# Performance work log

Measured on AMD Instinct MI355X. Metric: run time of the kernel, lower is better.

The kernel has to match this reference:

```python
import jax, jax.numpy as jnp
import numpy as np
from jax import lax

IMG = 224.0
IOU_THRESH = 0.5

def box_cxcywh_to_xyxy(b):
    cx, cy, w, h = b[..., 0], b[..., 1], b[..., 2], b[..., 3]
    return jnp.stack([cx - 0.5 * w, cy - 0.5 * h, cx + 0.5 * w, cy + 0.5 * h], axis=-1)

def box_iou(a, b):
    area_a = (a[:, 2] - a[:, 0]) * (a[:, 3] - a[:, 1])
    area_b = (b[:, 2] - b[:, 0]) * (b[:, 3] - b[:, 1])
    lt = jnp.maximum(a[:, None, :2], b[None, :, :2])
    rb = jnp.minimum(a[:, None, 2:], b[None, :, 2:])
    wh = jnp.clip(rb - lt, 0.0)
    inter = wh[..., 0] * wh[..., 1]
    return inter / (area_a[:, None] + area_b[None, :] - inter)

def gumbel_softmax(key, logits, axis, tau=1.0):
    # straight-through hard gumbel-softmax (matches torch hard=True)
    g = jax.random.gumbel(key, logits.shape, logits.dtype)
    y = jax.nn.softmax((logits + g) / tau, axis=axis)
    y_hard = jax.nn.one_hot(jnp.argmax(y, axis=axis), y.shape[axis], axis=axis, dtype=y.dtype)
    return y + lax.stop_gradient(y_hard - y)

def nms_indices(boxes, scores, thresh):
    # iterative greedy NMS, returns kept indices in descending-score order (as torchvision)
    n = boxes.shape[0]
    order = jnp.argsort(-scores)
    b = boxes[order]
    areas = (b[:, 2] - b[:, 0]) * (b[:, 3] - b[:, 1])
    pos = jnp.arange(n)
    def body(i, suppressed):
        bi = b[i]
        lt = jnp.maximum(bi[:2], b[:, :2])
        rb = jnp.minimum(bi[2:], b[:, 2:])
        wh = jnp.clip(rb - lt, 0.0)
        inter = wh[:, 0] * wh[:, 1]
        iou = inter / (areas[i] + areas - inter)
        sup = (iou > thresh) & (pos > i) & jnp.logical_not(suppressed[i])
        return suppressed | sup
    suppressed = lax.fori_loop(0, n, body, jnp.zeros((n,), bool))
    keep = np.asarray(jnp.logical_not(suppressed))
    return jnp.asarray(np.asarray(order)[keep])

def _keys():
    return jax.random.split(jax.random.key(42), 3)

def _boxes_and_scores(classencodings, pred_logits, pred_boxes, tgt_ids, batch_idx, tgt_bbox, k0):
    C = classencodings.shape[0]
    B, Q, D = pred_logits.shape
    similarity = jnp.einsum('bqd,cd->bqc', pred_logits, classencodings)
    out_scores = jnp.max(similarity, axis=-1)
    clt = gumbel_softmax(k0, similarity, axis=-1)                      # [B,Q,C] hard
    offx = jnp.arange(C, dtype=pred_logits.dtype) * IMG
    offy = jnp.arange(B, dtype=pred_logits.dtype) * IMG
    ox = jnp.sum(clt * offx, axis=-1)                                  # [B,Q]
    oy = jnp.broadcast_to(offy[:, None], (B, Q))
    out_off = jnp.tile(jnp.stack([ox, oy], axis=-1), (1, 1, 2))        # [B,Q,4]
    out_bbox = (box_cxcywh_to_xyxy(pred_boxes) + out_off).reshape(-1, 4)
    f = pred_logits.dtype
    gt_off = jnp.tile(jnp.stack([IMG * tgt_ids.astype(f), IMG * batch_idx.astype(f)], axis=-1), (1, 2))
    tb = box_cxcywh_to_xyxy(tgt_bbox) + gt_off                         # [N,4]
    return similarity, out_scores.reshape(-1), out_bbox, tb

def ce_diag(logits):
    # CrossEntropyLoss(mean) with targets arange(n)
    return -jnp.mean(jnp.diagonal(jax.nn.log_softmax(logits, axis=1)))

def _forward(classencodings, pred_logits, pred_boxes, pred_masks, tgt_masks, tgt_embs, tgt_bbox, tgt_ids, batch_idx, nms_idx):
    k0, k1, k2 = _keys()
    B, Q, D = pred_logits.shape
    N = tgt_embs.shape[0]
    W, H = tgt_masks.shape[-2:]
    similarity, out_scores, out_bbox, tb = _boxes_and_scores(classencodings, pred_logits, pred_boxes, tgt_ids, batch_idx, tgt_bbox, k0)
    kept = out_bbox[nms_idx]                                           # [K,4]
    K = kept.shape[0]
    iou = box_iou(kept, tb)
    iou = jnp.where(jnp.isnan(iou), 0.0, iou)
    gt_log = jax.nn.softmax(iou, axis=1)
    gt_one_hot = gumbel_softmax(k1, gt_log, axis=1)                    # [K,N]
    gt_sel = gt_one_hot.T @ kept                                       # [N,4]
    gt_ious = jnp.diagonal(box_iou(gt_sel, tb))
    out_embs = gt_one_hot.T @ pred_logits.reshape(-1, D)[nms_idx]      # [N,D]
    class_loss = ce_diag(tgt_embs @ out_embs.T) + ce_diag(out_embs @ tgt_embs.T)
    scores = jnp.einsum('bqd,nd->bqn', pred_logits, tgt_embs).reshape(B * Q, N)
    ind = gumbel_softmax(k2, scores, axis=0).T                         # [N,B*Q]
    om = (ind @ pred_masks.reshape(B * Q, -1)).reshape(N, W, H)
    overall_mask_loss = jnp.mean((om - tgt_masks) ** 2)
    ocm = jnp.einsum('qwh,bcq->bcwh', om, similarity) / om.shape[1]    # [B,Q,W,H] (N==C==Q)
    ocm = jax.nn.softmax(ocm, axis=1)
    batch_lookup = jax.nn.one_hot(batch_idx, B, dtype=pred_logits.dtype).T  # [B,N]
    gt_sim = tgt_embs @ classencodings.T                               # [N,C]
    tsim = batch_lookup[:, :, None] * gt_sim[None, :, :]               # [B,N,C]
    gt_cm = jnp.einsum('bnc,nwh->bcwh', tsim, tgt_masks)               # [B,C,W,H]
    inp = ocm.reshape(B, -1)
    tgt = gt_cm.reshape(B, -1)
    dice = jnp.mean(jnp.sum(inp * tgt) / (jnp.sum(inp, -1) + jnp.sum(tgt, -1) + 1e-6))
    l1 = jnp.abs(gt_sel - tb).sum()
    return jnp.stack([class_loss, dice, overall_mask_loss / K, (1.0 - gt_ious).sum() / K, l1 / K])

def setup_inputs():
    key = jax.random.key(0)
    ks = jax.random.split(key, 10)
    B, Q, C, N, D, W, H = 8, 300, 300, 300, 256, 96, 96
    return {
        'classencodings': jax.random.normal(ks[0], (C, D), jnp.float32),
        'pred_logits': jax.random.normal(ks[1], (B, Q, D), jnp.float32),
        'pred_boxes': jax.random.uniform(ks[2], (B, Q, 4), jnp.float32),
        'pred_masks': jax.random.normal(ks[3], (B * Q, W, H), jnp.float32),
        'tgt_masks': jax.random.uniform(ks[4], (N, W, H), jnp.float32),
        'tgt_embs': jax.random.normal(ks[5], (N, D), jnp.float32),
        'tgt_bbox': jax.random.uniform(ks[6], (N, 4), jnp.float32),
        'im_masks': jnp.ones((B, 224, 224), jnp.float32),
        'tgt_ids': jax.random.randint(ks[7], (N,), 0, C, jnp.int32),
        'batch_idx': jnp.sort(jax.random.randint(ks[8], (N,), 0, B, jnp.int32)),
    }

def reference(classencodings, pred_logits, pred_boxes, pred_masks, tgt_masks, tgt_embs, tgt_bbox, im_masks, tgt_ids, batch_idx):
    k0, _, _ = _keys()
    _, scores, out_bbox, _ = _boxes_and_scores(classencodings, pred_logits, pred_boxes, tgt_ids, batch_idx, tgt_bbox, k0)
    nms_idx = nms_indices(out_bbox, scores, IOU_THRESH)
    return _forward(classencodings, pred_logits, pred_boxes, pred_masks, tgt_masks, tgt_embs, tgt_bbox, tgt_ids, batch_idx, nms_idx)
```

## Files before the change

### kernel.cpp

```cpp
#include <hip/hip_runtime.h>
#include <stdint.h>

#define DEVFN __device__ __forceinline__

typedef unsigned short u16;
typedef short bf16x8 __attribute__((ext_vector_type(8)));
typedef float f32x4 __attribute__((ext_vector_type(4)));

constexpr int BB = 8, QQ = 300, CC = 300, NN = 300, DD = 256;
constexpr int WHX = 9216, BQ = 2400, SIMW = 600;
constexpr int QP = 320;
constexpr int CP = 304;
constexpr int KP = 96;
constexpr int NP = 416;
constexpr int CELLCAP = 300;

constexpr size_t F_SIMS   = 0;
constexpr size_t F_GTSIM  = F_SIMS   + (size_t)BQ*SIMW;
constexpr size_t F_MM     = F_GTSIM  + (size_t)NN*CC;
constexpr size_t F_SCORE  = F_MM     + (size_t)NN*NN;
constexpr size_t F_BBOX   = F_SCORE  + BQ;
constexpr size_t F_TB     = F_BBOX   + (size_t)BQ*4;
constexpr size_t F_SB     = F_TB     + (size_t)NN*4;
constexpr size_t F_SAREA  = F_SB     + (size_t)BQ*4;
constexpr size_t F_KB     = F_SAREA  + BQ;
constexpr size_t F_ROWSUM = F_KB     + (size_t)BQ*4;
constexpr size_t F_OE     = F_ROWSUM + NN;
constexpr size_t F_GSEL   = F_OE     + (size_t)NN*DD;
constexpr size_t F_MSUM   = F_GSEL   + (size_t)NN*4;
constexpr size_t F_STGT   = F_MSUM   + NN;
constexpr size_t F_SC     = F_STGT   + 8;
constexpr size_t F_CNT    = F_SC     + 16;
constexpr size_t F_ACCEND = F_CNT    + BQ;
constexpr size_t F_ORDER  = F_ACCEND;
constexpr size_t F_NMSIDX = F_ORDER  + BQ;
constexpr size_t F_SEL2   = F_NMSIDX + BQ;
constexpr size_t F_BSTART = F_SEL2   + NN;
constexpr size_t F_KINT   = F_BSTART + 16;
constexpr size_t F_CLS    = F_KINT   + 4;
constexpr size_t F_KEEPF  = F_CLS    + BQ;
constexpr size_t F_LIST   = F_KEEPF  + BQ;
constexpr size_t F_SIMTB  = ((F_LIST + (size_t)BQ*CELLCAP + 7) & ~(size_t)7);
constexpr size_t F_OMT    = F_SIMTB + (size_t)BB*CP*QP/2;
constexpr size_t F_TMT    = F_OMT   + (size_t)WHX*QP/2;
constexpr size_t F_GTP    = F_TMT   + (size_t)WHX*NP/2;
constexpr size_t F_TOTAL  = F_GTP   + (size_t)BB*CP*KP/2;

DEVFN uint32_t rotl32(uint32_t v, int r){ return (v << r) | (v >> (32 - r)); }

DEVFN void tf2x32(uint32_t k0, uint32_t k1, uint32_t x0, uint32_t x1,
                  uint32_t& o0, uint32_t& o1){
  uint32_t ks2 = k0 ^ k1 ^ 0x1BD11BDAu;
  x0 += k0; x1 += k1;
#define TFR(r) x0 += x1; x1 = rotl32(x1, r); x1 ^= x0;
  TFR(13) TFR(15) TFR(26) TFR(6)   x0 += k1;  x1 += ks2 + 1u;
  TFR(17) TFR(29) TFR(16) TFR(24)  x0 += ks2; x1 += k0  + 2u;
  TFR(13) TFR(15) TFR(26) TFR(6)   x0 += k0;  x1 += k1  + 3u;
  TFR(17) TFR(29) TFR(16) TFR(24)  x0 += k1;  x1 += ks2 + 4u;
  TFR(13) TFR(15) TFR(26) TFR(6)   x0 += ks2; x1 += k0  + 5u;
#undef TFR
  o0 = x0; o1 = x1;
}

DEVFN void subkey(int i, uint32_t& k0, uint32_t& k1){
  tf2x32(0u, 42u, 0u, (uint32_t)i, k0, k1);
}

DEVFN float gumbel32(uint32_t k0, uint32_t k1, uint32_t idx){
  uint32_t h, l; tf2x32(k0, k1, 0u, idx, h, l);
  uint32_t bits = h ^ l;
  float f = __uint_as_float((bits >> 9) | 0x3F800000u) - 1.0f;
  const float tiny = 1.17549435e-38f;
  float u = fmaxf(tiny, f + tiny);
  return -logf(-logf(u));
}

DEVFN float iou_xyxy(float ax1,float ay1,float ax2,float ay2,
                     float bx1,float by1,float bx2,float by2){
  float aa = (ax2-ax1)*(ay2-ay1);
  float ab = (bx2-bx1)*(by2-by1);
  float lx = fmaxf(ax1,bx1), ly = fmaxf(ay1,by1);
  float rx = fminf(ax2,bx2), ry = fminf(ay2,by2);
  float iw = fmaxf(rx-lx,0.f), ih = fmaxf(ry-ly,0.f);
  float in_ = iw*ih;
  return in_/(aa+ab-in_);
}

DEVFN u16 f2bf(float x){
  uint32_t u = __float_as_uint(x);
  uint32_t r = u + 0x7FFFu + ((u >> 16) & 1u);
  return (u16)(r >> 16);
}

__global__ __launch_bounds__(256) void k_gemm_t(
    const float* __restrict__ pl, const float* __restrict__ ce,
    const float* __restrict__ te, float* __restrict__ sims,
    float* __restrict__ gtsim){
  __shared__ float As[16][64];
  __shared__ float Bs[16][64];
  const int row0 = blockIdx.x * 64, col0 = blockIdx.y * 64;
  const int tid = threadIdx.x;
  const int lrow = tid >> 2, lk0 = (tid & 3) * 4;
  const int tr = tid >> 4, tc = tid & 15;

  float acc[4][4];
  #pragma unroll
  for (int i = 0; i < 4; i++)
    #pragma unroll
    for (int j = 0; j < 4; j++) acc[i][j] = 0.f;

  const float4 z4 = {0.f,0.f,0.f,0.f};
  const int grow = row0 + lrow;
  const int gcol = col0 + lrow;
  const float* arow = nullptr;
  if (grow < 2400) arow = pl + (size_t)grow * DD;
  else if (grow < 2700) arow = te + (size_t)(grow - 2400) * DD;
  const float* brow = nullptr;
  if (gcol < 300) brow = ce + (size_t)gcol * DD;
  else if (gcol < 600) brow = te + (size_t)(gcol - 300) * DD;

  float4 av = arow ? *(const float4*)(arow + lk0) : z4;
  float4 bv = brow ? *(const float4*)(brow + lk0) : z4;

  for (int step = 0; step < 16; step++){
    __syncthreads();
    #pragma unroll
    for (int j = 0; j < 4; j++){
      As[lk0 + j][lrow] = ((const float*)&av)[j];
      Bs[lk0 + j][lrow] = ((const float*)&bv)[j];
    }
    __syncthreads();
    if (step + 1 < 16){
      const int k0 = (step + 1) * 16;
      av = arow ? *(const float4*)(arow + k0 + lk0) : z4;
      bv = brow ? *(const float4*)(brow + k0 + lk0) : z4;
    }
    #pragma unroll
    for (int kk = 0; kk < 16; kk++){
      float4 a4 = *(const float4*)&As[kk][tr*4];
      float4 b4 = *(const float4*)&Bs[kk][tc*4];
      float a[4] = {a4.x,a4.y,a4.z,a4.w};
      float b[4] = {b4.x,b4.y,b4.z,b4.w};
      #pragma unroll
      for (int i = 0; i < 4; i++)
        #pragma unroll
        for (int j = 0; j < 4; j++)
          acc[i][j] = fmaf(a[i], b[j], acc[i][j]);
    }
  }

  #pragma unroll
  for (int i = 0; i < 4; i++){
    const int r = row0 + tr*4 + i;
    const int c0 = col0 + tc*4;
    if (r < 2400){
      if (c0 < 600){
        float4 o0 = {acc[i][0],acc[i][1],acc[i][2],acc[i][3]};
        *(float4*)(sims + (size_t)r*SIMW + c0) = o0;
      }
    } else if (r < 2700){
      const int n = r - 2400;
      #pragma unroll
      for (int j = 0; j < 4; j++){
        int c = c0 + j;
        if (c < 300) gtsim[(size_t)n*CC + c] = acc[i][j];
      }
    }
  }
}

__global__ __launch_bounds__(512) void k_post(
    const float* __restrict__ sims, const float* __restrict__ pb,
    const float* __restrict__ tbb, const int* __restrict__ tids,
    const int* __restrict__ bidx, const float* __restrict__ gtsim,
    float* __restrict__ score, float* __restrict__ bbox,
    float* __restrict__ tb, float* __restrict__ rowsum,
    int* __restrict__ clsout){
  int bq = blockIdx.x, tid = threadIdx.x;
  __shared__ float sv[512];
  __shared__ int   si[512];
  float v = (tid < CC) ? sims[(size_t)bq*SIMW + tid] : -INFINITY;
  sv[tid] = v; __syncthreads();
  for (int s = 256; s > 0; s >>= 1){ if (tid < s) sv[tid] = fmaxf(sv[tid], sv[tid+s]); __syncthreads(); }
  if (tid == 0) score[bq] = sv[0];
  __syncthreads();
  uint32_t gk0, gk1; subkey(0, gk0, gk1);
  float y = (tid < CC) ? v + gumbel32(gk0, gk1, (uint32_t)(bq*CC + tid)) : -INFINITY;
  sv[tid] = y; si[tid] = tid; __syncthreads();
  for (int s = 256; s > 0; s >>= 1){
    if (tid < s){
      float ov = sv[tid+s]; int oi = si[tid+s];
      if (ov > sv[tid] || (ov == sv[tid] && oi < si[tid])){ sv[tid] = ov; si[tid] = oi; }
    }
    __syncthreads();
  }
  if (tid == 0){
    int cls = si[0];
    clsout[bq] = cls;
    float ox = 224.0f * (float)cls;
    float oy = 224.0f * (float)(bq / QQ);
    float cx = pb[bq*4+0], cy = pb[bq*4+1], ww = pb[bq*4+2], hh = pb[bq*4+3];
    bbox[bq*4+0] = cx - 0.5f*ww + ox;
    bbox[bq*4+1] = cy - 0.5f*hh + oy;
    bbox[bq*4+2] = cx + 0.5f*ww + ox;
    bbox[bq*4+3] = cy + 0.5f*hh + oy;
  }
  if (bq < NN){
    __syncthreads();
    float rs = (tid < CC) ? gtsim[(size_t)bq*CC + tid] : 0.f;
    sv[tid] = rs; __syncthreads();
    for (int s = 256; s > 0; s >>= 1){ if (tid < s) sv[tid] += sv[tid+s]; __syncthreads(); }
    if (tid == 0) rowsum[bq] = sv[0];
    if (tid == 1){
      float gx = 224.0f * (float)tids[bq], gy = 224.0f * (float)bidx[bq];
      float cx = tbb[bq*4+0], cy = tbb[bq*4+1], ww = tbb[bq*4+2], hh = tbb[bq*4+3];
      tb[bq*4+0] = cx - 0.5f*ww + gx;
      tb[bq*4+1] = cy - 0.5f*hh + gy;
      tb[bq*4+2] = cx + 0.5f*ww + gx;
      tb[bq*4+3] = cy + 0.5f*hh + gy;
    }
  }
}

__global__ __launch_bounds__(256) void k_rank(
    const float* __restrict__ score, int* __restrict__ order){
  const int t = blockIdx.x;
  const int tid = threadIdx.x;
  const float st = score[t];
  int cnt = 0;
  for (int j = tid; j < BQ; j += 256){
    float sj = score[j];
    cnt += (sj > st) || (sj == st && j < t);
  }
  __shared__ int red[256];
  red[tid] = cnt; __syncthreads();
  for (int s = 128; s > 0; s >>= 1){
    if (tid < s) red[tid] += red[tid+s];
    __syncthreads();
  }
  if (tid == 0) order[red[0]] = t;
}

__global__ __launch_bounds__(256) void k_gather(
    const float* __restrict__ bbox, const int* __restrict__ order,
    const int* __restrict__ bidx, const int* __restrict__ cls,
    float* __restrict__ sb, float* __restrict__ sarea,
    int* __restrict__ bstart, int* __restrict__ cnt,
    int* __restrict__ list){
  int t = blockIdx.x*256 + threadIdx.x;
  if (t < BQ){
    int o = order[t];
    float x1 = bbox[o*4+0], y1 = bbox[o*4+1], x2 = bbox[o*4+2], y2 = bbox[o*4+3];
    sb[t*4+0] = x1; sb[t*4+1] = y1; sb[t*4+2] = x2; sb[t*4+3] = y2;
    sarea[t] = (x2-x1)*(y2-y1);
    int key = (o / QQ) * CC + cls[o];
    int slot = atomicAdd(&cnt[key], 1);
    list[(size_t)key*CELLCAP + slot] = t;
  }
  if (blockIdx.x == 0 && threadIdx.x < 9){
    int b = threadIdx.x, c = 0;
    for (int n = 0; n < NN; n++) c += (bidx[n] < b);
    bstart[b] = c;
  }
}

__global__ __launch_bounds__(256) void k_cellnms(
    const float* __restrict__ sb, const int* __restrict__ cnt,
    const int* __restrict__ list, int* __restrict__ keepf){
  int key = blockIdx.x*256 + threadIdx.x;
  if (key >= BB*CC) return;
  int m = cnt[key];
  if (m <= 0) return;
  const int* lst = list + (size_t)key*CELLCAP;
  unsigned long long keptmask = 0ull;
  int prevp = -1;
  for (int a = 0; a < m; a++){
    int pa = 0x7fffffff;
    for (int j = 0; j < m; j++){
      int pj = lst[j];
      if (pj > prevp && pj < pa) pa = pj;
    }
    prevp = pa;
    float4 A = ((const float4*)sb)[pa];
    float areaA = (A.z-A.x)*(A.w-A.y);
    bool kept = true;
    int pbprev = -1;
    for (int b2 = 0; b2 < a; b2++){
      int pb = 0x7fffffff;
      for (int j = 0; j < m; j++){
        int pj = lst[j];
        if (pj > pbprev && pj < pb) pb = pj;
      }
      pbprev = pb;
      bool keptb = (m <= 64) ? (((keptmask >> b2) & 1ull) != 0ull) : (keepf[pb] != 0);
      if (!keptb) continue;
      float4 B = ((const float4*)sb)[pb];
      float areaB = (B.z-B.x)*(B.w-B.y);
      float lx = fmaxf(A.x,B.x), ly = fmaxf(A.y,B.y);
      float rx = fminf(A.z,B.z), ry = fminf(A.w,B.w);
      float iw = fmaxf(rx-lx,0.f), ih = fmaxf(ry-ly,0.f);
      float inter = iw*ih;
      if (inter/(areaA + areaB - inter) > 0.5f){ kept = false; break; }
    }
    if (m <= 64 && kept) keptmask |= (1ull << a);
    keepf[pa] = kept ? 1 : 0;
  }
}

__global__ __launch_bounds__(256) void k_compact(
    const int* __restrict__ keepflag, const int* __restrict__ order,
    const float* __restrict__ sb, int* __restrict__ nmsidx,
    float* __restrict__ kb, int* __restrict__ kint){
  __shared__ int csum[256];
  int tid = threadIdx.x;
  int p0 = tid*10;
  int keepf[10];
  int cnt = 0;
  #pragma unroll
  for (int d = 0; d < 10; d++){
    int p = p0 + d;
    int k = 0;
    if (p < BQ) k = keepflag[p];
    keepf[d] = k; cnt += k;
  }
  csum[tid] = cnt; __syncthreads();
  for (int s = 1; s < 256; s <<= 1){
    int add = (tid >= s) ? csum[tid - s] : 0;
    __syncthreads();
    csum[tid] += add;
    __syncthreads();
  }
  int pos = csum[tid] - cnt;
  #pragma unroll
  for (int d = 0; d < 10; d++){
    if (keepf[d]){
      int p = p0 + d;
      nmsidx[pos] = order[p];
      ((float4*)kb)[pos] = ((const float4*)sb)[p];
      pos++;
    }
  }
  if (tid == 255) kint[0] = csum[255];
}

__global__ __launch_bounds__(512) void k_gtsel(
    const float* __restrict__ kb, const float* __restrict__ tb,
    const int* __restrict__ nmsidx, const float* __restrict__ pl,
    const int* __restrict__ kint, float* __restrict__ gsel,
    float* __restrict__ oe){
  int k = blockIdx.x;
  if (k >= kint[0]) return;
  int tid = threadIdx.x;
  __shared__ float sv[512];
  __shared__ int   si[512];
  float4 a = ((const float4*)kb)[k];
  float iou = -INFINITY;
  if (tid < NN){
    float4 t = ((const float4*)tb)[tid];
    iou = iou_xyxy(a.x,a.y,a.z,a.w, t.x,t.y,t.z,t.w);
    if (iou != iou) iou = 0.f;
  }
  sv[tid] = iou; __syncthreads();
  for (int s = 256; s > 0; s >>= 1){ if (tid < s) sv[tid] = fmaxf(sv[tid], sv[tid+s]); __syncthreads(); }
  float m = sv[0]; __syncthreads();
  float e = (tid < NN) ? expf(iou - m) : 0.f;
  sv[tid] = e; __syncthreads();
  for (int s = 256; s > 0; s >>= 1){ if (tid < s) sv[tid] += sv[tid+s]; __syncthreads(); }
  float S = sv[0]; __syncthreads();
  uint32_t gk0, gk1; subkey(1, gk0, gk1);
  float y = (tid < NN) ? (e / S + gumbel32(gk0, gk1, (uint32_t)(k*NN + tid))) : -INFINITY;
  sv[tid] = y; si[tid] = tid; __syncthreads();
  for (int s = 256; s > 0; s >>= 1){
    if (tid < s){
      float ov = sv[tid+s]; int oi = si[tid+s];
      if (ov > sv[tid] || (ov == sv[tid] && oi < si[tid])){ sv[tid] = ov; si[tid] = oi; }
    }
    __syncthreads();
  }
  int sel = si[0];
  if (tid < 4) atomicAdd(&gsel[sel*4 + tid], ((const float*)&a)[tid]);
  if (tid < DD) atomicAdd(&oe[(size_t)sel*DD + tid], pl[(size_t)nmsidx[k]*DD + tid]);
}

__global__ __launch_bounds__(512) void k_gtiou(
    const float* __restrict__ gsel, const float* __restrict__ tb,
    float* __restrict__ sc){
  int tid = threadIdx.x;
  __shared__ float s1[512], s2[512];
  float a1 = 0.f, a2 = 0.f;
  if (tid < NN){
    float4 g = ((const float4*)gsel)[tid];
    float4 t = ((const float4*)tb)[tid];
    float iou = iou_xyxy(g.x,g.y,g.z,g.w, t.x,t.y,t.z,t.w);
    a1 = 1.f - iou;
    a2 = fabsf(g.x-t.x) + fabsf(g.y-t.y) + fabsf(g.z-t.z) + fabsf(g.w-t.w);
  }
  s1[tid] = a1; s2[tid] = a2; __syncthreads();
  for (int s = 256; s > 0; s >>= 1){
    if (tid < s){ s1[tid] += s1[tid+s]; s2[tid] += s2[tid+s]; }
    __syncthreads();
  }
  if (tid == 0){ sc[3] = s1[0]; sc[4] = s2[0]; }
}

__global__ __launch_bounds__(256) void k_m(
    const float* __restrict__ te, const float* __restrict__ oe,
    float* __restrict__ M){
  int idx = blockIdx.x*256 + threadIdx.x;
  if (idx >= NN*NN) return;
  int i = idx / NN, j = idx % NN;
  const float4* a4 = (const float4*)(te + (size_t)i*DD);
  const float4* b4 = (const float4*)(oe + (size_t)j*DD);
  float s = 0.f;
  #pragma unroll 8
  for (int t = 0; t < DD/4; t++){
    float4 x = a4[t], y = b4[t];
    s += x.x*y.x + x.y*y.y + x.z*y.z + x.w*y.w;
  }
  M[idx] = s;
}

__global__ __launch_bounds__(64) void k_ce(
    const float* __restrict__ M, float* __restrict__ sc){
  int i = blockIdx.x, lane = threadIdx.x;
  float m = -INFINITY;
  for (int j = lane; j < NN; j += 64) m = fmaxf(m, M[(size_t)i*NN + j]);
  for (int o = 32; o > 0; o >>= 1) m = fmaxf(m, __shfl_xor(m, o));
  float s = 0.f;
  for (int j = lane; j < NN; j += 64) s += expf(M[(size_t)i*NN + j] - m);
  for (int o = 32; o > 0; o >>= 1) s += __shfl_xor(s, o);
  float lr = m + logf(s);
  float m2 = -INFINITY;
  for (int j = lane; j < NN; j += 64) m2 = fmaxf(m2, M[(size_t)j*NN + i]);
  for (int o = 32; o > 0; o >>= 1) m2 = fmaxf(m2, __shfl_xor(m2, o));
  float s2 = 0.f;
  for (int j = lane; j < NN; j += 64) s2 += expf(M[(size_t)j*NN + i] - m2);
  for (int o = 32; o > 0; o >>= 1) s2 += __shfl_xor(s2, o);
  float lc = m2 + logf(s2);
  if (lane == 0){
    float d = M[(size_t)i*NN + i];
    atomicAdd(&sc[0], lr - d);
    atomicAdd(&sc[1], lc - d);
  }
}

__global__ __launch_bounds__(256) void k_sel2(
    const float* __restrict__ sims, int* __restrict__ sel2){
  int n = blockIdx.x, tid = threadIdx.x;
  uint32_t gk0, gk1; subkey(2, gk0, gk1);
  float best = -INFINITY; int bi = 0x7fffffff;
  for (int r = tid; r < BQ; r += 256){
    float v = sims[(size_t)r*SIMW + CC + n] + gumbel32(gk0, gk1, (uint32_t)(r*NN + n));
    if (v > best){ best = v; bi = r; }
  }
  __shared__ float sv[256];
  __shared__ int   si[256];
  sv[tid] = best; si[tid] = bi; __syncthreads();
  for (int s = 128; s > 0; s >>= 1){
    if (tid < s){
      float ov = sv[tid+s]; int oi = si[tid+s];
      if (ov > sv[tid] || (ov == sv[tid] && oi < si[tid])){ sv[tid] = ov; si[tid] = oi; }
    }
    __syncthreads();
  }
  if (tid == 0) sel2[n] = si[0];
}

__global__ __launch_bounds__(256) void k_om(
    const float* __restrict__ pm, const float* __restrict__ tm,
    const int* __restrict__ sel2, float* __restrict__ msum,
    float* __restrict__ sc){
  int nb = blockIdx.x;
  int n = nb / 9, ch = nb % 9;
  int c0 = ch*1024 + threadIdx.x*4;
  const float4 o4 = *(const float4*)(pm + (size_t)sel2[n]*WHX + c0);
  const float4 t4 = *(const float4*)(tm + (size_t)n*WHX + c0);
  float dx = o4.x-t4.x, dy = o4.y-t4.y, dz = o4.z-t4.z, dw = o4.w-t4.w;
  float d2 = dx*dx + dy*dy + dz*dz + dw*dw;
  float ts = t4.x + t4.y + t4.z + t4.w;
  __shared__ float r1[256], r2[256];
  r1[threadIdx.x] = d2; r2[threadIdx.x] = ts; __syncthreads();
  for (int s = 128; s > 0; s >>= 1){
    if (threadIdx.x < s){ r1[threadIdx.x] += r1[threadIdx.x+s]; r2[threadIdx.x] += r2[threadIdx.x+s]; }
    __syncthreads();
  }
  if (threadIdx.x == 0){ atomicAdd(&sc[2], r1[0]); atomicAdd(&msum[n], r2[0]); }
}

__global__ __launch_bounds__(512) void k_sumtgt(
    const int* __restrict__ bidx, const float* __restrict__ rowsum,
    const float* __restrict__ msum, float* __restrict__ stgt){
  int n = threadIdx.x;
  if (n >= NN) return;
  atomicAdd(&stgt[bidx[n]], rowsum[n] * msum[n]);
}

__global__ __launch_bounds__(256) void t_simT(
    const float* __restrict__ sims, u16* __restrict__ simTb){
  __shared__ float ld[32][65];
  int q0 = blockIdx.x*32, c0 = blockIdx.y*64, b = blockIdx.z;
  int tid = threadIdx.x;
  for (int i = tid; i < 32*64; i += 256){
    int qi = i >> 6, ci = i & 63;
    int q = q0 + qi, c = c0 + ci;
    ld[qi][ci] = (q < QQ && c < CC) ? sims[((size_t)b*QQ + q)*SIMW + c] : 0.f;
  }
  __syncthreads();
  int cloc = tid >> 2, j0 = (tid & 3)*8;
  int c = c0 + cloc;
  if (c < CP){
    u16 tmp[8];
    #pragma unroll
    for (int j = 0; j < 8; j++) tmp[j] = f2bf(ld[j0+j][cloc]);
    *(uint4*)(simTb + ((size_t)b*CP + c)*QP + q0 + j0) = *(const uint4*)tmp;
  }
}

__global__ __launch_bounds__(256) void t_omT(
    const float* __restrict__ pm, const int* __restrict__ sel2,
    u16* __restrict__ omT){
  __shared__ float ld[32][65];
  int q0 = blockIdx.x*32, wh0 = blockIdx.y*64;
  int tid = threadIdx.x;
  for (int i = tid; i < 32*64; i += 256){
    int qi = i >> 6, wi = i & 63;
    int q = q0 + qi;
    ld[qi][wi] = (q < QQ) ? pm[(size_t)sel2[q]*WHX + wh0 + wi] * (1.0f/96.0f) : 0.f;
  }
  __syncthreads();
  int wloc = tid >> 2, j0 = (tid & 3)*8;
  u16 tmp[8];
  #pragma unroll
  for (int j = 0; j < 8; j++) tmp[j] = f2bf(ld[j0+j][wloc]);
  *(uint4*)(omT + (size_t)(wh0+wloc)*QP + q0 + j0) = *(const uint4*)tmp;
}

__global__ __launch_bounds__(256) void t_tmT(
    const float* __restrict__ tm, u16* __restrict__ tmT){
  __shared__ float ld[32][65];
  int n0 = blockIdx.x*32, wh0 = blockIdx.y*64;
  int tid = threadIdx.x;
  for (int i = tid; i < 32*64; i += 256){
    int ni = i >> 6, wi = i & 63;
    int n = n0 + ni;
    ld[ni][wi] = (n < NN) ? tm[(size_t)n*WHX + wh0 + wi] : 0.f;
  }
  __syncthreads();
  int wloc = tid >> 2, j0 = (tid & 3)*8;
  u16 tmp[8];
  #pragma unroll
  for (int j = 0; j < 8; j++) tmp[j] = f2bf(ld[j0+j][wloc]);
  *(uint4*)(tmT + (size_t)(wh0+wloc)*NP + n0 + j0) = *(const uint4*)tmp;
}

__global__ __launch_bounds__(256) void t_gtp(
    const float* __restrict__ gtsim, const int* __restrict__ bstart,
    u16* __restrict__ gtp){
  int g = blockIdx.x*256 + threadIdx.x;
  if (g >= BB*CP*(KP/8)) return;
  int b = g / (CP*(KP/8));
  int rem = g - b*(CP*(KP/8));
  int c = rem / (KP/8);
  int kg = rem % (KP/8);
  int n0 = bstart[b], n1 = bstart[b+1];
  int kst = n0 & ~7;
  u16 tmp[8];
  #pragma unroll
  for (int j = 0; j < 8; j++){
    int n = kst + kg*8 + j;
    float v = (n >= n0 && n < n1 && c < CC) ? gtsim[(size_t)n*CC + c] : 0.f;
    tmp[j] = f2bf(v);
  }
  *(uint4*)(gtp + ((size_t)b*CP + c)*KP + kg*8) = *(const uint4*)tmp;
}

constexpr int ALDS = 32;
__global__ __launch_bounds__(256) void k_zsoft(
    const u16* __restrict__ simTb, const u16* __restrict__ omT,
    const u16* __restrict__ gtp, const u16* __restrict__ tmT,
    const int* __restrict__ bstart, float* __restrict__ sc){
  const int bid = blockIdx.x;
  const int xcd = bid & 7;
  const int r9  = bid >> 3;
  const int tile = xcd * 18 + (r9 % 18);
  const int b    = r9 / 18;
  const int tid = threadIdx.x;
  const int w = tid >> 6, l = tid & 63;
  const int lrow = l & 15, lgrp = l >> 4;
  const int col = tile*64 + w*16 + lrow;

  __shared__ u16 As[CP*ALDS];
  __shared__ float red[256];

  const u16* Ab = simTb + (size_t)b*CP*QP;
  const int sidx[5] = {tid, tid+256, tid+512, tid+768, tid+1024};
  int woff[5];
  #pragma unroll
  for (int i = 0; i < 5; i++){
    int rr = sidx[i] >> 2, g = sidx[i] & 3;
    woff[i] = rr*ALDS + ((g ^ ((rr >> 1) & 3)) << 3);
  }
  const int roff = (lgrp ^ ((lrow >> 1) & 3)) << 3;

  uint4 pf0, pf1, pf2, pf3, pf4;
  {
    int rr, g;
    rr = sidx[0] >> 2; g = sidx[0] & 3; pf0 = *(const uint4*)(Ab + (size_t)rr*QP + g*8);
    rr = sidx[1] >> 2; g = sidx[1] & 3; pf1 = *(const uint4*)(Ab + (size_t)rr*QP + g*8);
    rr = sidx[2] >> 2; g = sidx[2] & 3; pf2 = *(const uint4*)(Ab + (size_t)rr*QP + g*8);
    rr = sidx[3] >> 2; g = sidx[3] & 3; pf3 = *(const uint4*)(Ab + (size_t)rr*QP + g*8);
    if (sidx[4] < 1216){ rr = sidx[4] >> 2; g = sidx[4] & 3; pf4 = *(const uint4*)(Ab + (size_t)rr*QP + g*8); }
  }
  const u16* pB = omT + (size_t)col*QP;
  bf16x8 bcur = *(const bf16x8*)(pB);

  f32x4 acc[19];
  #pragma unroll
  for (int t = 0; t < 19; t++) acc[t] = (f32x4){0.f,0.f,0.f,0.f};

  for (int ks = 0; ks < 10; ks++){
    *(uint4*)&As[woff[0]] = pf0;
    *(uint4*)&As[woff[1]] = pf1;
    *(uint4*)&As[woff[2]] = pf2;
    *(uint4*)&As[woff[3]] = pf3;
    if (sidx[4] < 1216) *(uint4*)&As[woff[4]] = pf4;
    __syncthreads();
    bf16x8 bnext;
    if (ks + 1 < 10){
      const size_t ko = (size_t)(ks + 1) * 32;
      int rr, g;
      rr = sidx[0] >> 2; g = sidx[0] & 3; pf0 = *(const uint4*)(Ab + (size_t)rr*QP + ko + g*8);
      rr = sidx[1] >> 2; g = sidx[1] & 3; pf1 = *(const uint4*)(Ab + (size_t)rr*QP + ko + g*8);
      rr = sidx[2] >> 2; g = sidx[2] & 3; pf2 = *(const uint4*)(Ab + (size_t)rr*QP + ko + g*8);
      rr = sidx[3] >> 2; g = sidx[3] & 3; pf3 = *(const uint4*)(Ab + (size_t)rr*QP + ko + g*8);
      if (sidx[4] < 1216){ rr = sidx[4] >> 2; g = sidx[4] & 3; pf4 = *(const uint4*)(Ab + (size_t)rr*QP + ko + g*8); }
      bnext = *(const bf16x8*)(pB + ko);
    }
    #pragma unroll
    for (int t = 0; t < 19; t++){
      bf16x8 af = *(const bf16x8*)&As[t*16*ALDS + lrow*ALDS + roff];
      acc[t] = __builtin_amdgcn_mfma_f32_16x16x32_bf16(af, bcur, acc[t], 0, 0, 0);
    }
    bcur = bnext;
    __syncthreads();
  }

  float lmax = -INFINITY;
  #pragma unroll
  for (int t = 0; t < 19; t++){
    if (t == 18 && lgrp == 3) continue;
    lmax = fmaxf(lmax, fmaxf(fmaxf(acc[t][0], acc[t][1]), fmaxf(acc[t][2], acc[t][3])));
  }
  lmax = fmaxf(lmax, __shfl_xor(lmax, 16));
  lmax = fmaxf(lmax, __shfl_xor(lmax, 32));
  float ls = 0.f;
  #pragma unroll
  for (int t = 0; t < 19; t++){
    if (t == 18 && lgrp == 3){
      acc[t] = (f32x4){0.f,0.f,0.f,0.f};
      continue;
    }
    float p0 = __expf(acc[t][0] - lmax);
    float p1 = __expf(acc[t][1] - lmax);
    float p2 = __expf(acc[t][2] - lmax);
    float p3 = __expf(acc[t][3] - lmax);
    acc[t][0] = p0; acc[t][1] = p1; acc[t][2] = p2; acc[t][3] = p3;
    ls += p0 + p1 + p2 + p3;
  }
  float S = ls;
  S += __shfl_xor(S, 16);
  S += __shfl_xor(S, 32);
  float inv = 1.f / S;

  int n0 = bstart[b];
  int kst = n0 & ~7;
  const u16* tB = tmT + (size_t)col*NP + kst + lgrp*8;
  bf16x8 b2a = *(const bf16x8*)(tB);
  bf16x8 b2b = *(const bf16x8*)(tB + 32);
  bf16x8 b2c = *(const bf16x8*)(tB + 64);
  const u16* A2 = gtp + (size_t)b*CP*KP + lgrp*8;
  float dl = 0.f;
  #pragma unroll
  for (int t = 0; t < 19; t++){
    const u16* ar = A2 + (size_t)(t*16 + lrow)*KP;
    f32x4 rr = (f32x4){0.f,0.f,0.f,0.f};
    rr = __builtin_amdgcn_mfma_f32_16x16x32_bf16(*(const bf16x8*)(ar),      b2a, rr, 0, 0, 0);
    rr = __builtin_amdgcn_mfma_f32_16x16x32_bf16(*(const bf16x8*)(ar + 32), b2b, rr, 0, 0, 0);
    rr = __builtin_amdgcn_mfma_f32_16x16x32_bf16(*(const bf16x8*)(ar + 64), b2c, rr, 0, 0, 0);
    dl += acc[t][0]*rr[0] + acc[t][1]*rr[1] + acc[t][2]*rr[2] + acc[t][3]*rr[3];
  }
  dl *= inv;

  red[tid] = dl; __syncthreads();
  for (int s = 128; s > 0; s >>= 1){
    if (tid < s) red[tid] += red[tid+s];
    __syncthreads();
  }
  if (tid == 0) atomicAdd(&sc[5], red[0]);
}

__global__ __launch_bounds__(64) void k_final(
    const float* __restrict__ sc, const float* __restrict__ stgt,
    const int* __restrict__ kint, float* __restrict__ out){
  if (threadIdx.x != 0) return;
  float K = (float)kint[0];
  float cls = sc[0]/300.f + sc[1]/300.f;
  float stot = sc[5];
  float dice = 0.f;
  for (int b = 0; b < 8; b++) dice += stot / (9216.0f + stgt[b] + 1e-6f);
  dice *= (1.0f/8.0f);
  out[0] = cls;
  out[1] = dice;
  out[2] = (sc[2] / 2764800.0f) / K;
  out[3] = sc[3] / K;
  out[4] = sc[4] / K;
}

extern "C" void kernel_launch(void* const* d_in, const int* in_sizes, int n_in,
                              void* d_out, int out_size, void* d_ws, size_t ws_size,
                              hipStream_t stream) {
  const float* ce  = (const float*)d_in[0];
  const float* pl  = (const float*)d_in[1];
  const float* pb  = (const float*)d_in[2];
  const float* pm  = (const float*)d_in[3];
  const float* tm  = (const float*)d_in[4];
  const float* te  = (const float*)d_in[5];
  const float* tbb = (const float*)d_in[6];
  const int*  tids = (const int*)d_in[8];
  const int*  bidx = (const int*)d_in[9];
  float* out = (float*)d_out;
  float* w = (float*)d_ws;

  if (ws_size < F_TOTAL * sizeof(float)) return;

  float* SIMS   = w + F_SIMS;
  float* GTSIM  = w + F_GTSIM;
  float* MM     = w + F_MM;
  float* SCORE  = w + F_SCORE;
  float* BBOX   = w + F_BBOX;
  float* TBOX   = w + F_TB;
  float* SB     = w + F_SB;
  float* SAREA  = w + F_SAREA;
  float* KB     = w + F_KB;
  float* ROWSUM = w + F_ROWSUM;
  float* OE     = w + F_OE;
  float* GSEL   = w + F_GSEL;
  float* MSUM   = w + F_MSUM;
  float* STGT   = w + F_STGT;
  float* SC     = w + F_SC;
  int*   CNT    = (int*)(w + F_CNT);
  int*   ORDER  = (int*)(w + F_ORDER);
  int*   NMSIDX = (int*)(w + F_NMSIDX);
  int*   SEL2   = (int*)(w + F_SEL2);
  int*   BSTART = (int*)(w + F_BSTART);
  int*   KINT   = (int*)(w + F_KINT);
  int*   CLS    = (int*)(w + F_CLS);
  int*   KEEPF  = (int*)(w + F_KEEPF);
  int*   LIST   = (int*)(w + F_LIST);
  u16* SIMTB = (u16*)(w + F_SIMTB);
  u16* OMT   = (u16*)(w + F_OMT);
  u16* TMT   = (u16*)(w + F_TMT);
  u16* GTP   = (u16*)(w + F_GTP);

  hipMemsetAsync(w + F_OE, 0, (F_ACCEND - F_OE) * sizeof(float), stream);

  k_gemm_t<<<dim3(43, 10), 256, 0, stream>>>(pl, ce, te, SIMS, GTSIM);
  k_post<<<BQ, 512, 0, stream>>>(SIMS, pb, tbb, tids, bidx, GTSIM, SCORE, BBOX, TBOX, ROWSUM, CLS);
  k_rank<<<BQ, 256, 0, stream>>>(SCORE, ORDER);
  k_gather<<<(BQ + 255)/256, 256, 0, stream>>>(BBOX, ORDER, bidx, CLS, SB, SAREA, BSTART, CNT, LIST);
  k_cellnms<<<(BB*CC + 255)/256, 256, 0, stream>>>(SB, CNT, LIST, KEEPF);
  k_compact<<<1, 256, 0, stream>>>(KEEPF, ORDER, SB, NMSIDX, KB, KINT);
  k_gtsel<<<BQ, 512, 0, stream>>>(KB, TBOX, NMSIDX, pl, KINT, GSEL, OE);
  k_gtiou<<<1, 512, 0, stream>>>(GSEL, TBOX, SC);
  k_m<<<(NN*NN + 255)/256, 256, 0, stream>>>(te, OE, MM);
  k_ce<<<NN, 64, 0, stream>>>(MM, SC);
  k_sel2<<<NN, 256, 0, stream>>>(SIMS, SEL2);
  k_om<<<NN*9, 256, 0, stream>>>(pm, tm, SEL2, MSUM, SC);
  k_sumtgt<<<1, 512, 0, stream>>>(bidx, ROWSUM, MSUM, STGT);

  t_simT<<<dim3(QP/32, 5, BB), 256, 0, stream>>>(SIMS, SIMTB);
  t_omT<<<dim3(QP/32, WHX/64), 256, 0, stream>>>(pm, SEL2, OMT);
  t_tmT<<<dim3(NP/32, WHX/64), 256, 0, stream>>>(tm, TMT);
  t_gtp<<<(BB*CP*(KP/8) + 255)/256, 256, 0, stream>>>(GTSIM, BSTART, GTP);

  k_zsoft<<<dim3((WHX/64) * BB), 256, 0, stream>>>(SIMTB, OMT, GTP, TMT, BSTART, SC);
  k_final<<<1, 64, 0, stream>>>(SC, STGT, KINT, out);
}
```

Baseline: 280.6 us.

## Fuse rank/gather and tail kernels; double-buffer zsoft A tile via direct LDS loads

Result: faster. 274.1 us (-2.3%).

```diff
diff --git a/kernel.cpp b/kernel.cpp
--- a/kernel.cpp
+++ b/kernel.cpp
@@ -92,6 +92,13 @@
   return (u16)(r >> 16);
 }
 
+DEVFN void gload_lds16(const u16* g, u16* l){
+  __builtin_amdgcn_global_load_lds(
+      (const __attribute__((address_space(1))) unsigned int*)g,
+      (__attribute__((address_space(3))) unsigned int*)l,
+      16, 0, 0);
+}
+
 __global__ __launch_bounds__(256) void k_gemm_t(
     const float* __restrict__ pl, const float* __restrict__ ce,
     const float* __restrict__ te, float* __restrict__ sims,
@@ -222,45 +229,39 @@
   }
 }
 
-__global__ __launch_bounds__(256) void k_rank(
-    const float* __restrict__ score, int* __restrict__ order){
+__global__ __launch_bounds__(256) void k_rankgather(
+    const float* __restrict__ score, const float* __restrict__ bbox,
+    const int* __restrict__ cls, const int* __restrict__ bidx,
+    int* __restrict__ order, float* __restrict__ sb,
+    int* __restrict__ bstart, int* __restrict__ cnt,
+    int* __restrict__ list){
   const int t = blockIdx.x;
   const int tid = threadIdx.x;
   const float st = score[t];
-  int cnt = 0;
+  int c = 0;
   for (int j = tid; j < BQ; j += 256){
     float sj = score[j];
-    cnt += (sj > st) || (sj == st && j < t);
+    c += (sj > st) || (sj == st && j < t);
   }
   __shared__ int red[256];
-  red[tid] = cnt; __syncthreads();
+  red[tid] = c; __syncthreads();
   for (int s = 128; s > 0; s >>= 1){
     if (tid < s) red[tid] += red[tid+s];
     __syncthreads();
   }
-  if (tid == 0) order[red[0]] = t;
-}
-
-__global__ __launch_bounds__(256) void k_gather(
-    const float* __restrict__ bbox, const int* __restrict__ order,
-    const int* __restrict__ bidx, const int* __restrict__ cls,
-    float* __restrict__ sb, float* __restrict__ sarea,
-    int* __restrict__ bstart, int* __restrict__ cnt,
-    int* __restrict__ list){
-  int t = blockIdx.x*256 + threadIdx.x;
-  if (t < BQ){
-    int o = order[t];
-    float x1 = bbox[o*4+0], y1 = bbox[o*4+1], x2 = bbox[o*4+2], y2 = bbox[o*4+3];
-    sb[t*4+0] = x1; sb[t*4+1] = y1; sb[t*4+2] = x2; sb[t*4+3] = y2;
-    sarea[t] = (x2-x1)*(y2-y1);
-    int key = (o / QQ) * CC + cls[o];
+  if (tid == 0){
+    int r = red[0];
+    order[r] = t;
+    float x1 = bbox[t*4+0], y1 = bbox[t*4+1], x2 = bbox[t*4+2], y2 = bbox[t*4+3];
+    sb[r*4+0] = x1; sb[r*4+1] = y1; sb[r*4+2] = x2; sb[r*4+3] = y2;
+    int key = (t / QQ) * CC + cls[t];
     int slot = atomicAdd(&cnt[key], 1);
-    list[(size_t)key*CELLCAP + slot] = t;
-  }
-  if (blockIdx.x == 0 && threadIdx.x < 9){
-    int b = threadIdx.x, c = 0;
-    for (int n = 0; n < NN; n++) c += (bidx[n] < b);
-    bstart[b] = c;
+    list[(size_t)key*CELLCAP + slot] = r;
+  }
+  if (t == 0 && tid >= 32 && tid < 41){
+    int b = tid - 32, cb = 0;
+    for (int n = 0; n < NN; n++) cb += (bidx[n] < b);
+    bstart[b] = cb;
   }
 }
 
@@ -382,27 +383,6 @@
   if (tid < DD) atomicAdd(&oe[(size_t)sel*DD + tid], pl[(size_t)nmsidx[k]*DD + tid]);
 }
 
-__global__ __launch_bounds__(512) void k_gtiou(
-    const float* __restrict__ gsel, const float* __restrict__ tb,
-    float* __restrict__ sc){
-  int tid = threadIdx.x;
-  __shared__ float s1[512], s2[512];
-  float a1 = 0.f, a2 = 0.f;
-  if (tid < NN){
-    float4 g = ((const float4*)gsel)[tid];
-    float4 t = ((const float4*)tb)[tid];
-    float iou = iou_xyxy(g.x,g.y,g.z,g.w, t.x,t.y,t.z,t.w);
-    a1 = 1.f - iou;
-    a2 = fabsf(g.x-t.x) + fabsf(g.y-t.y) + fabsf(g.z-t.z) + fabsf(g.w-t.w);
-  }
-  s1[tid] = a1; s2[tid] = a2; __syncthreads();
-  for (int s = 256; s > 0; s >>= 1){
-    if (tid < s){ s1[tid] += s1[tid+s]; s2[tid] += s2[tid+s]; }
-    __syncthreads();
-  }
-  if (tid == 0){ sc[3] = s1[0]; sc[4] = s2[0]; }
-}
-
 __global__ __launch_bounds__(256) void k_m(
     const float* __restrict__ te, const float* __restrict__ oe,
     float* __restrict__ M){
@@ -487,14 +467,6 @@
   if (threadIdx.x == 0){ atomicAdd(&sc[2], r1[0]); atomicAdd(&msum[n], r2[0]); }
 }
 
-__global__ __launch_bounds__(512) void k_sumtgt(
-    const int* __restrict__ bidx, const float* __restrict__ rowsum,
-    const float* __restrict__ msum, float* __restrict__ stgt){
-  int n = threadIdx.x;
-  if (n >= NN) return;
-  atomicAdd(&stgt[bidx[n]], rowsum[n] * msum[n]);
-}
-
 __global__ __launch_bounds__(256) void t_simT(
     const float* __restrict__ sims, u16* __restrict__ simTb){
   __shared__ float ld[32][65];
@@ -589,58 +561,51 @@
   const int lrow = l & 15, lgrp = l >> 4;
   const int col = tile*64 + w*16 + lrow;
 
-  __shared__ u16 As[CP*ALDS];
+  __shared__ u16 As[2][CP*ALDS];
   __shared__ float red[256];
 
   const u16* Ab = simTb + (size_t)b*CP*QP;
-  const int sidx[5] = {tid, tid+256, tid+512, tid+768, tid+1024};
-  int woff[5];
+  int srcoff[5];
   #pragma unroll
   for (int i = 0; i < 5; i++){
-    int rr = sidx[i] >> 2, g = sidx[i] & 3;
-    woff[i] = rr*ALDS + ((g ^ ((rr >> 1) & 3)) << 3);
-  }
+    int p = (w*5 + i)*64 + l;
+    int row = p >> 2, cs = p & 3;
+    int g = cs ^ ((row >> 1) & 3);
+    srcoff[i] = row*QP + g*8;
+  }
+  const int nIss = (w == 3) ? 4 : 5;
   const int roff = (lgrp ^ ((lrow >> 1) & 3)) << 3;
-
-  uint4 pf0, pf1, pf2, pf3, pf4;
-  {
-    int rr, g;
-    rr = sidx[0] >> 2; g = sidx[0] & 3; pf0 = *(const uint4*)(Ab + (size_t)rr*QP + g*8);
-    rr = sidx[1] >> 2; g = sidx[1] & 3; pf1 = *(const uint4*)(Ab + (size_t)rr*QP + g*8);
-    rr = sidx[2] >> 2; g = sidx[2] & 3; pf2 = *(const uint4*)(Ab + (size_t)rr*QP + g*8);
-    rr = sidx[3] >> 2; g = sidx[3] & 3; pf3 = *(const uint4*)(Ab + (size_t)rr*QP + g*8);
-    if (sidx[4] < 1216){ rr = sidx[4] >> 2; g = sidx[4] & 3; pf4 = *(const uint4*)(Ab + (size_t)rr*QP + g*8); }
-  }
   const u16* pB = omT + (size_t)col*QP;
+
+  #pragma unroll
+  for (int i = 0; i < 5; i++){
+    if (i < nIss) gload_lds16(Ab + srcoff[i], &As[0][(w*5+i)*512]);
+  }
   bf16x8 bcur = *(const bf16x8*)(pB);
 
   f32x4 acc[19];
   #pragma unroll
   for (int t = 0; t < 19; t++) acc[t] = (f32x4){0.f,0.f,0.f,0.f};
+  __syncthreads();
 
   for (int ks = 0; ks < 10; ks++){
-    *(uint4*)&As[woff[0]] = pf0;
-    *(uint4*)&As[woff[1]] = pf1;
-    *(uint4*)&As[woff[2]] = pf2;
-    *(uint4*)&As[woff[3]] = pf3;
-    if (sidx[4] < 1216) *(uint4*)&As[woff[4]] = pf4;
-    __syncthreads();
+    const int cur = ks & 1;
     bf16x8 bnext;
     if (ks + 1 < 10){
-      const size_t ko = (size_t)(ks + 1) * 32;
-      int rr, g;
-      rr = sidx[0] >> 2; g = sidx[0] & 3; pf0 = *(const uint4*)(Ab + (size_t)rr*QP + ko + g*8);
-      rr = sidx[1] >> 2; g = sidx[1] & 3; pf1 = *(const uint4*)(Ab + (size_t)rr*QP + ko + g*8);
-      rr = sidx[2] >> 2; g = sidx[2] & 3; pf2 = *(const uint4*)(Ab + (size_t)rr*QP + ko + g*8);
-      rr = sidx[3] >> 2; g = sidx[3] & 3; pf3 = *(const uint4*)(Ab + (size_t)rr*QP + ko + g*8);
-      if (sidx[4] < 1216){ rr = sidx[4] >> 2; g = sidx[4] & 3; pf4 = *(const uint4*)(Ab + (size_t)rr*QP + ko + g*8); }
+      const int ko = (ks + 1) * 32;
+      #pragma unroll
+      for (int i = 0; i < 5; i++){
+        if (i < nIss) gload_lds16(Ab + srcoff[i] + ko, &As[cur ^ 1][(w*5+i)*512]);
+      }
       bnext = *(const bf16x8*)(pB + ko);
     }
+    __builtin_amdgcn_s_setprio(1);
     #pragma unroll
     for (int t = 0; t < 19; t++){
-      bf16x8 af = *(const bf16x8*)&As[t*16*ALDS + lrow*ALDS + roff];
+      bf16x8 af = *(const bf16x8*)&As[cur][t*16*ALDS + lrow*ALDS + roff];
       acc[t] = __builtin_amdgcn_mfma_f32_16x16x32_bf16(af, bcur, acc[t], 0, 0, 0);
     }
+    __builtin_amdgcn_s_setprio(0);
     bcur = bnext;
     __syncthreads();
   }
@@ -699,21 +664,43 @@
   if (tid == 0) atomicAdd(&sc[5], red[0]);
 }
 
-__global__ __launch_bounds__(64) void k_final(
-    const float* __restrict__ sc, const float* __restrict__ stgt,
+__global__ __launch_bounds__(512) void k_final3(
+    const float* __restrict__ gsel, const float* __restrict__ tb,
+    const int* __restrict__ bidx, const float* __restrict__ rowsum,
+    const float* __restrict__ msum, const float* __restrict__ sc,
     const int* __restrict__ kint, float* __restrict__ out){
-  if (threadIdx.x != 0) return;
-  float K = (float)kint[0];
-  float cls = sc[0]/300.f + sc[1]/300.f;
-  float stot = sc[5];
-  float dice = 0.f;
-  for (int b = 0; b < 8; b++) dice += stot / (9216.0f + stgt[b] + 1e-6f);
-  dice *= (1.0f/8.0f);
-  out[0] = cls;
-  out[1] = dice;
-  out[2] = (sc[2] / 2764800.0f) / K;
-  out[3] = sc[3] / K;
-  out[4] = sc[4] / K;
+  int tid = threadIdx.x;
+  __shared__ float s1[512], s2[512];
+  __shared__ float stgt[8];
+  if (tid < 8) stgt[tid] = 0.f;
+  __syncthreads();
+  float a1 = 0.f, a2 = 0.f;
+  if (tid < NN){
+    float4 g = ((const float4*)gsel)[tid];
+    float4 t = ((const float4*)tb)[tid];
+    float iou = iou_xyxy(g.x,g.y,g.z,g.w, t.x,t.y,t.z,t.w);
+    a1 = 1.f - iou;
+    a2 = fabsf(g.x-t.x) + fabsf(g.y-t.y) + fabsf(g.z-t.z) + fabsf(g.w-t.w);
+    atomicAdd(&stgt[bidx[tid]], rowsum[tid] * msum[tid]);
+  }
+  s1[tid] = a1; s2[tid] = a2; __syncthreads();
+  for (int s = 256; s > 0; s >>= 1){
+    if (tid < s){ s1[tid] += s1[tid+s]; s2[tid] += s2[tid+s]; }
+    __syncthreads();
+  }
+  if (tid == 0){
+    float K = (float)kint[0];
+    float cls = sc[0]/300.f + sc[1]/300.f;
+    float stot = sc[5];
+    float dice = 0.f;
+    for (int b = 0; b < 8; b++) dice += stot / (9216.0f + stgt[b] + 1e-6f);
+    dice *= (1.0f/8.0f);
+    out[0] = cls;
+    out[1] = dice;
+    out[2] = (sc[2] / 2764800.0f) / K;
+    out[3] = s1[0] / K;
+    out[4] = s2[0] / K;
+  }
 }
 
 extern "C" void kernel_launch(void* const* d_in, const int* in_sizes, int n_in,
@@ -740,13 +727,11 @@
   float* BBOX   = w + F_BBOX;
   float* TBOX   = w + F_TB;
   float* SB     = w + F_SB;
-  float* SAREA  = w + F_SAREA;
   float* KB     = w + F_KB;
   float* ROWSUM = w + F_ROWSUM;
   float* OE     = w + F_OE;
   float* GSEL   = w + F_GSEL;
   float* MSUM   = w + F_MSUM;
-  float* STGT   = w + F_STGT;
   float* SC     = w + F_SC;
   int*   CNT    = (int*)(w + F_CNT);
   int*   ORDER  = (int*)(w + F_ORDER);
@@ -766,17 +751,14 @@
 
   k_gemm_t<<<dim3(43, 10), 256, 0, stream>>>(pl, ce, te, SIMS, GTSIM);
   k_post<<<BQ, 512, 0, stream>>>(SIMS, pb, tbb, tids, bidx, GTSIM, SCORE, BBOX, TBOX, ROWSUM, CLS);
-  k_rank<<<BQ, 256, 0, stream>>>(SCORE, ORDER);
-  k_gather<<<(BQ + 255)/256, 256, 0, stream>>>(BBOX, ORDER, bidx, CLS, SB, SAREA, BSTART, CNT, LIST);
+  k_rankgather<<<BQ, 256, 0, stream>>>(SCORE, BBOX, CLS, bidx, ORDER, SB, BSTART, CNT, LIST);
   k_cellnms<<<(BB*CC + 255)/256, 256, 0, stream>>>(SB, CNT, LIST, KEEPF);
   k_compact<<<1, 256, 0, stream>>>(KEEPF, ORDER, SB, NMSIDX, KB, KINT);
   k_gtsel<<<BQ, 512, 0, stream>>>(KB, TBOX, NMSIDX, pl, KINT, GSEL, OE);
-  k_gtiou<<<1, 512, 0, stream>>>(GSEL, TBOX, SC);
   k_m<<<(NN*NN + 255)/256, 256, 0, stream>>>(te, OE, MM);
   k_ce<<<NN, 64, 0, stream>>>(MM, SC);
   k_sel2<<<NN, 256, 0, stream>>>(SIMS, SEL2);
   k_om<<<NN*9, 256, 0, stream>>>(pm, tm, SEL2, MSUM, SC);
-  k_sumtgt<<<1, 512, 0, stream>>>(bidx, ROWSUM, MSUM, STGT);
 
   t_simT<<<dim3(QP/32, 5, BB), 256, 0, stream>>>(SIMS, SIMTB);
   t_omT<<<dim3(QP/32, WHX/64), 256, 0, stream>>>(pm, SEL2, OMT);
@@ -784,5 +766,5 @@
   t_gtp<<<(BB*CP*(KP/8) + 255)/256, 256, 0, stream>>>(GTSIM, BSTART, GTP);
 
   k_zsoft<<<dim3((WHX/64) * BB), 256, 0, stream>>>(SIMTB, OMT, GTP, TMT, BSTART, SC);
-  k_final<<<1, 64, 0, stream>>>(SC, STGT, KINT, out);
-}
+  k_final3<<<1, 512, 0, stream>>>(GSEL, TBOX, bidx, ROWSUM, MSUM, SC, KINT, out);
+}
```
